# Performance work log

Measured on AMD Instinct MI355X. Metric: run time of the kernel, lower is better.

The kernel has to match this reference:

```python
import jax, jax.numpy as jnp
import numpy as np

N_TETS = 200000
IN_FEATURES = 128
OUT_FEATURES = 128
NUM_NEIGHBORS = 4  # NEIGHBORHOOD_SIZE = 5 = self + 4 neighbors


def setup_inputs() -> dict:
    key = jax.random.key(0)
    k1, k2, k3, k4 = jax.random.split(key, 4)
    features = jax.random.normal(k1, (N_TETS, IN_FEATURES), dtype=jnp.float32)
    neighbors = jax.random.randint(k2, (N_TETS, NUM_NEIGHBORS), 0, N_TETS, dtype=jnp.int64)
    # torch nn.Linear convention: W is [out_features, 5*in_features]
    fan_in = (1 + NUM_NEIGHBORS) * IN_FEATURES
    bound = 1.0 / np.sqrt(fan_in)
    W = jax.random.uniform(k3, (OUT_FEATURES, fan_in), minval=-bound, maxval=bound, dtype=jnp.float32)
    b = jax.random.uniform(k4, (OUT_FEATURES,), minval=-bound, maxval=bound, dtype=jnp.float32)
    return {"features": features, "neighbors": neighbors, "W": W, "b": b}


def reference(features, neighbors, W, b):
    # Gather neighbor features: [N, 4, F]
    nbr_feats = features[neighbors]
    N = features.shape[0]
    # Concat self + 4 neighbors along feature dim -> [N, 5F]
    stacked = jnp.concatenate([features[:, None, :], nbr_feats], axis=1).reshape(N, -1)
    # Linear + ReLU (torch: x @ W.T + b)
    return jax.nn.relu(stacked @ W.T + b)
```

## Files before the change

### kernel.cpp

```cpp
#include <hip/hip_runtime.h>
#include <stdint.h>

#define NTETS   200000
#define FEATS   128
#define OUTF    128
#define NG      5
#define BM      128
#define NTHR    512
#define NBLOCKS ((NTETS + BM - 1) / BM)
#define SUBS    10
#define SUBW    16384

typedef __attribute__((ext_vector_type(8))) short  short8v;
typedef __attribute__((ext_vector_type(4))) float  f32x4;

static __device__ __forceinline__ unsigned short bf16_rne(float f) {
  union { float f; unsigned u; } v; v.f = f;
  unsigned r = v.u + 0x7FFFu + ((v.u >> 16) & 1u);
  return (unsigned short)(r >> 16);
}

static __device__ __forceinline__ void gload_lds16(const void* g, void* l) {
  __builtin_amdgcn_global_load_lds(
      (const __attribute__((address_space(1))) unsigned int*)g,
      (__attribute__((address_space(3))) unsigned int*)l, 16, 0, 0);
}

__global__ void detect_mode_k(const int* __restrict__ nbr, int* __restrict__ flag) {
  int t = threadIdx.x;
  int nz = 0;
  for (int i = t; i < 4096; i += 64) nz |= nbr[2 * i + 1];
  unsigned long long any = __ballot(nz != 0);
  if (t == 0) flag[0] = (any == 0ULL) ? 1 : 0;
}

__global__ void prep_wfrag_k(const float* __restrict__ W, unsigned short* __restrict__ wf) {
  int id = blockIdx.x * 256 + threadIdx.x;
  if (id >= NG * 16384) return;
  int e  = id & 7;
  int l6 = (id >> 3) & 63;
  int ns = (id >> 9) & 7;
  int kk = (id >> 12) & 3;
  int g  = id >> 14;
  int n = ns * 16 + (l6 & 15);
  int k = g * 128 + kk * 32 + (l6 >> 4) * 8 + e;
  wf[id] = bf16_rne(W[n * (NG * FEATS) + k]);
}

__global__ __launch_bounds__(256) void prep_f_k(const float* __restrict__ feat,
                                                unsigned short* __restrict__ fimg) {
  size_t i = ((size_t)blockIdx.x * 256 + threadIdx.x) * 8;
  f32x4 a = __builtin_nontemporal_load((const f32x4*)(feat + i));
  f32x4 b = __builtin_nontemporal_load((const f32x4*)(feat + i + 4));
  short8v v;
  v[0] = (short)bf16_rne(a[0]); v[1] = (short)bf16_rne(a[1]);
  v[2] = (short)bf16_rne(a[2]); v[3] = (short)bf16_rne(a[3]);
  v[4] = (short)bf16_rne(b[0]); v[5] = (short)bf16_rne(b[1]);
  v[6] = (short)bf16_rne(b[2]); v[7] = (short)bf16_rne(b[3]);
  *(short8v*)(fimg + i) = v;
}

__global__ __launch_bounds__(NTHR, 4) void conv_k(
    const unsigned short* __restrict__ fimg, const int* __restrict__ nbr,
    const float* __restrict__ bias, const unsigned short* __restrict__ wf,
    const int* __restrict__ mode, float* __restrict__ out)
{
  __shared__ __align__(16) char wtile[3][SUBW];
  __shared__ unsigned srcoff[NG][BM];

  const int t    = threadIdx.x;
  const int row0 = blockIdx.x * BM;
  const int lane = t & 63;
  const int wv   = t >> 6;
  const int lr   = lane & 15;
  const int lk   = lane >> 4;

  {
    const bool m64 = (mode[0] != 0);
    for (int e = t; e < NG * BM; e += NTHR) {
      int g = e >> 7, r = e & (BM - 1);
      int gr = row0 + r;
      int s = 0;
      if (gr < NTETS) {
        if (g == 0) s = gr;
        else {
          size_t idx = (size_t)gr * 4 + (g - 1);
          s = m64 ? nbr[2 * idx] : nbr[idx];
          if ((unsigned)s >= (unsigned)NTETS) s = 0;
        }
      }
      srcoff[g][r] = (unsigned)s * 256u;
    }
  }
  __syncthreads();

  const char* fimgc = (const char*)fimg;
  const char* aptr[NG];
#pragma unroll
  for (int g = 0; g < NG; ++g)
    aptr[g] = fimgc + srcoff[g][wv * 16 + lr] + (unsigned)(lk * 16);

  const f32x4 zero = {0.f, 0.f, 0.f, 0.f};
  f32x4 acc[8];
#pragma unroll
  for (int i = 0; i < 8; ++i) acc[i] = zero;

  short8v a[4][2];

#define SB() __builtin_amdgcn_sched_barrier(0)

#define A_LOAD(dst_, p_, IMM_)                                                   \
  asm volatile("global_load_dwordx4 %0, %1, off offset:" #IMM_                   \
               : "=v"(dst_) : "v"(p_) : "memory")

#define A_ISSUE(ss) do {                                                         \
    const char* p_ = aptr[(ss) >> 1];                                            \
    if (((ss) & 1) == 0) {                                                       \
      A_LOAD(a[(ss) & 3][0], p_, 0);                                             \
      A_LOAD(a[(ss) & 3][1], p_, 64);                                            \
    } else {                                                                     \
      A_LOAD(a[(ss) & 3][0], p_, 128);                                           \
      A_LOAD(a[(ss) & 3][1], p_, 192);                                           \
    }                                                                            \
  } while (0)

#define W_ISSUE(ss) do {                                                         \
    const char* ws_ = (const char*)wf + (size_t)(ss) * SUBW + wv * 2048 +        \
                      (lane << 4);                                               \
    char* wd_ = &wtile[(ss) % 3][wv * 2048];                                     \
    gload_lds16(ws_, wd_);                                                       \
    gload_lds16(ws_ + 1024, wd_ + 1024);                                         \
  } while (0)

  W_ISSUE(0); SB();
  A_ISSUE(0); SB();
  W_ISSUE(1); SB();
  A_ISSUE(1); SB();
  A_ISSUE(2); SB();
  asm volatile("s_waitcnt vmcnt(6)" ::: "memory");
  SB();
  __builtin_amdgcn_s_barrier();
  SB();

#pragma unroll
  for (int s = 0; s < SUBS; ++s) {
    if (s + 2 < SUBS) { W_ISSUE(s + 2); SB(); }
    if (s + 3 < SUBS) { A_ISSUE(s + 3); SB(); }

    {
      short8v b[8];
#pragma unroll
      for (int ns = 0; ns < 8; ++ns)
        b[ns] = *(const short8v*)(&wtile[s % 3][ns * 1024 + (lane << 4)]);
#pragma unroll
      for (int ns = 0; ns < 8; ++ns)
        acc[ns] = __builtin_amdgcn_mfma_f32_16x16x32_bf16(a[s & 3][0], b[ns], acc[ns], 0, 0, 0);
#pragma unroll
      for (int ns = 0; ns < 8; ++ns)
        b[ns] = *(const short8v*)(&wtile[s % 3][(8 + ns) * 1024 + (lane << 4)]);
#pragma unroll
      for (int ns = 0; ns < 8; ++ns)
        acc[ns] = __builtin_amdgcn_mfma_f32_16x16x32_bf16(a[s & 3][1], b[ns], acc[ns], 0, 0, 0);
    }
    SB();

    if (s <= 6)      { asm volatile("s_waitcnt vmcnt(6)" ::: "memory"); }
    else if (s == 7) { asm volatile("s_waitcnt vmcnt(4)" ::: "memory"); }
    else if (s == 8) { asm volatile("s_waitcnt vmcnt(0)" ::: "memory"); }
    if (s + 1 < SUBS) {
      SB();
      __builtin_amdgcn_s_barrier();
      SB();
    }
  }

#pragma unroll
  for (int ns = 0; ns < 8; ++ns) {
    const int col = ns * 16 + lr;
    const float bv = bias[col];
    const int rbase = row0 + wv * 16 + lk * 4;
#pragma unroll
    for (int i = 0; i < 4; ++i) {
      int r = rbase + i;
      if (r < NTETS) {
        float vv = acc[ns][i] + bv;
        vv = vv > 0.f ? vv : 0.f;
        __builtin_nontemporal_store(vv, &out[(size_t)r * OUTF + col]);
      }
    }
  }
#undef A_LOAD
#undef A_ISSUE
#undef W_ISSUE
#undef SB
}

extern "C" void kernel_launch(void* const* d_in, const int* in_sizes, int n_in,
                              void* d_out, int out_size, void* d_ws, size_t ws_size,
                              hipStream_t stream) {
  const float* feat = (const float*)d_in[0];
  const int*   nbr  = (const int*)d_in[1];
  const float* W    = (const float*)d_in[2];
  const float* bias = (const float*)d_in[3];
  float* out = (float*)d_out;

  int* mode = (int*)d_ws;
  unsigned short* wf   = (unsigned short*)((char*)d_ws + 1024);
  unsigned short* fimg = (unsigned short*)((char*)d_ws + 164864);

  detect_mode_k<<<1, 64, 0, stream>>>(nbr, mode);
  prep_wfrag_k<<<320, 256, 0, stream>>>(W, wf);
  prep_f_k<<<(NTETS * FEATS / 8 + 255) / 256, 256, 0, stream>>>(feat, fimg);
  conv_k<<<NBLOCKS, NTHR, 0, stream>>>(fimg, nbr, bias, wf, mode, out);
}
```

Before: 118.7 us.

## Double per-wave row tile to reuse LDS weight fragments and drop A prefetch pipeline

Raises the block tile from 128 to 256 rows, so each wave computes two 16-row M sub-tiles and every weight fragment read from LDS feeds two MFMAs. This halves the block count and the total weight staging traffic. The hand-scheduled asm prefetch of activation rows, three sub-steps ahead, is removed. Gathered feature rows are now loaded with plain C++ loads inside the compute loop, which may expose gather latency since the vmcnt waits now count only the weight loads. Register pressure also rises with the doubled accumulators, against the launch bound of 4 blocks.

```diff
diff --git a/kernel.cpp b/kernel.cpp
--- a/kernel.cpp
+++ b/kernel.cpp
@@ -5,7 +5,7 @@
 #define FEATS   128
 #define OUTF    128
 #define NG      5
-#define BM      128
+#define BM      256
 #define NTHR    512
 #define NBLOCKS ((NTETS + BM - 1) / BM)
 #define SUBS    10
@@ -78,7 +78,7 @@
   {
     const bool m64 = (mode[0] != 0);
     for (int e = t; e < NG * BM; e += NTHR) {
-      int g = e >> 7, r = e & (BM - 1);
+      int g = e / BM, r = e & (BM - 1);
       int gr = row0 + r;
       int s = 0;
       if (gr < NTETS) {
@@ -95,34 +95,21 @@
   __syncthreads();
 
   const char* fimgc = (const char*)fimg;
-  const char* aptr[NG];
-#pragma unroll
-  for (int g = 0; g < NG; ++g)
-    aptr[g] = fimgc + srcoff[g][wv * 16 + lr] + (unsigned)(lk * 16);
+  unsigned aoff[2][NG];
+#pragma unroll
+  for (int m = 0; m < 2; ++m)
+#pragma unroll
+    for (int g = 0; g < NG; ++g)
+      aoff[m][g] = srcoff[g][wv * 32 + m * 16 + lr] + (unsigned)(lk * 16);
 
   const f32x4 zero = {0.f, 0.f, 0.f, 0.f};
-  f32x4 acc[8];
-#pragma unroll
-  for (int i = 0; i < 8; ++i) acc[i] = zero;
-
-  short8v a[4][2];
+  f32x4 acc[2][8];
+#pragma unroll
+  for (int m = 0; m < 2; ++m)
+#pragma unroll
+    for (int i = 0; i < 8; ++i) acc[m][i] = zero;
 
 #define SB() __builtin_amdgcn_sched_barrier(0)
-
-#define A_LOAD(dst_, p_, IMM_)                                                   \
-  asm volatile("global_load_dwordx4 %0, %1, off offset:" #IMM_                   \
-               : "=v"(dst_) : "v"(p_) : "memory")
-
-#define A_ISSUE(ss) do {                                                         \
-    const char* p_ = aptr[(ss) >> 1];                                            \
-    if (((ss) & 1) == 0) {                                                       \
-      A_LOAD(a[(ss) & 3][0], p_, 0);                                             \
-      A_LOAD(a[(ss) & 3][1], p_, 64);                                            \
-    } else {                                                                     \
-      A_LOAD(a[(ss) & 3][0], p_, 128);                                           \
-      A_LOAD(a[(ss) & 3][1], p_, 192);                                           \
-    }                                                                            \
-  } while (0)
 
 #define W_ISSUE(ss) do {                                                         \
     const char* ws_ = (const char*)wf + (size_t)(ss) * SUBW + wv * 2048 +        \
@@ -133,11 +120,8 @@
   } while (0)
 
   W_ISSUE(0); SB();
-  A_ISSUE(0); SB();
   W_ISSUE(1); SB();
-  A_ISSUE(1); SB();
-  A_ISSUE(2); SB();
-  asm volatile("s_waitcnt vmcnt(6)" ::: "memory");
+  asm volatile("s_waitcnt vmcnt(2)" ::: "memory");
   SB();
   __builtin_amdgcn_s_barrier();
   SB();
@@ -145,28 +129,35 @@
 #pragma unroll
   for (int s = 0; s < SUBS; ++s) {
     if (s + 2 < SUBS) { W_ISSUE(s + 2); SB(); }
-    if (s + 3 < SUBS) { A_ISSUE(s + 3); SB(); }
-
-    {
-      short8v b[8];
-#pragma unroll
-      for (int ns = 0; ns < 8; ++ns)
-        b[ns] = *(const short8v*)(&wtile[s % 3][ns * 1024 + (lane << 4)]);
-#pragma unroll
-      for (int ns = 0; ns < 8; ++ns)
-        acc[ns] = __builtin_amdgcn_mfma_f32_16x16x32_bf16(a[s & 3][0], b[ns], acc[ns], 0, 0, 0);
-#pragma unroll
-      for (int ns = 0; ns < 8; ++ns)
-        b[ns] = *(const short8v*)(&wtile[s % 3][(8 + ns) * 1024 + (lane << 4)]);
-#pragma unroll
-      for (int ns = 0; ns < 8; ++ns)
-        acc[ns] = __builtin_amdgcn_mfma_f32_16x16x32_bf16(a[s & 3][1], b[ns], acc[ns], 0, 0, 0);
+
+    const char* wt = wtile[s % 3];
+    const unsigned koff = (unsigned)((s & 1) * 128);
+#pragma unroll
+    for (int kk = 0; kk < 2; ++kk) {
+      short8v a0 = *(const short8v*)(fimgc + aoff[0][s >> 1] + koff + kk * 64);
+      short8v a1 = *(const short8v*)(fimgc + aoff[1][s >> 1] + koff + kk * 64);
+      short8v b4[4];
+#pragma unroll
+      for (int ns = 0; ns < 4; ++ns)
+        b4[ns] = *(const short8v*)(&wt[(kk * 8 + ns) * 1024 + (lane << 4)]);
+#pragma unroll
+      for (int ns = 0; ns < 4; ++ns) {
+        acc[0][ns] = __builtin_amdgcn_mfma_f32_16x16x32_bf16(a0, b4[ns], acc[0][ns], 0, 0, 0);
+        acc[1][ns] = __builtin_amdgcn_mfma_f32_16x16x32_bf16(a1, b4[ns], acc[1][ns], 0, 0, 0);
+      }
+#pragma unroll
+      for (int ns = 0; ns < 4; ++ns)
+        b4[ns] = *(const short8v*)(&wt[(kk * 8 + 4 + ns) * 1024 + (lane << 4)]);
+#pragma unroll
+      for (int ns = 0; ns < 4; ++ns) {
+        acc[0][4 + ns] = __builtin_amdgcn_mfma_f32_16x16x32_bf16(a0, b4[ns], acc[0][4 + ns], 0, 0, 0);
+        acc[1][4 + ns] = __builtin_amdgcn_mfma_f32_16x16x32_bf16(a1, b4[ns], acc[1][4 + ns], 0, 0, 0);
+      }
     }
     SB();
 
-    if (s <= 6)      { asm volatile("s_waitcnt vmcnt(6)" ::: "memory"); }
-    else if (s == 7) { asm volatile("s_waitcnt vmcnt(4)" ::: "memory"); }
-    else if (s == 8) { asm volatile("s_waitcnt vmcnt(0)" ::: "memory"); }
+    if (s + 2 < SUBS)      { asm volatile("s_waitcnt vmcnt(2)" ::: "memory"); }
+    else if (s + 1 < SUBS) { asm volatile("s_waitcnt vmcnt(0)" ::: "memory"); }
     if (s + 1 < SUBS) {
       SB();
       __builtin_amdgcn_s_barrier();
@@ -175,22 +166,23 @@
   }
 
 #pragma unroll
-  for (int ns = 0; ns < 8; ++ns) {
-    const int col = ns * 16 + lr;
-    const float bv = bias[col];
-    const int rbase = row0 + wv * 16 + lk * 4;
-#pragma unroll
-    for (int i = 0; i < 4; ++i) {
-      int r = rbase + i;
-      if (r < NTETS) {
-        float vv = acc[ns][i] + bv;
-        vv = vv > 0.f ? vv : 0.f;
-        __builtin_nontemporal_store(vv, &out[(size_t)r * OUTF + col]);
+  for (int m = 0; m < 2; ++m) {
+#pragma unroll
+    for (int ns = 0; ns < 8; ++ns) {
+      const int col = ns * 16 + lr;
+      const float bv = bias[col];
+      const int rbase = row0 + wv * 32 + m * 16 + lk * 4;
+#pragma unroll
+      for (int i = 0; i < 4; ++i) {
+        int r = rbase + i;
+        if (r < NTETS) {
+          float vv = acc[m][ns][i] + bv;
+          vv = vv > 0.f ? vv : 0.f;
+          __builtin_nontemporal_store(vv, &out[(size_t)r * OUTF + col]);
+        }
       }
     }
   }
-#undef A_LOAD
-#undef A_ISSUE
 #undef W_ISSUE
 #undef SB
 }
```

After: 113.7 us. 1.04x faster.

## Use persistent conv blocks with atomic tile counter and merge prep kernels

Applied to the files above, without the earlier changes.

Replaces the one-block-per-tile grid with 768 persistent blocks that take 128-row tiles from a global atomic counter. The mode-detection kernel is merged into the weight-fragment prep kernel, which also resets the counter, so one launch goes away. The explicit asm-pipelined A-operand gathers (prefetched three stages ahead) become plain loads issued just before each MFMA stage, and the occupancy hint rises from 4 to 6 blocks per CU. The aim is better load balance and less launch and tail overhead, but the A gather latency is no longer hidden by software prefetch, and each tile adds an atomic plus an extra barrier.

```diff
diff --git a/kernel.cpp b/kernel.cpp
--- a/kernel.cpp
+++ b/kernel.cpp
@@ -7,7 +7,8 @@
 #define NG      5
 #define BM      128
 #define NTHR    512
-#define NBLOCKS ((NTETS + BM - 1) / BM)
+#define NTILES  ((NTETS + BM - 1) / BM)
+#define NPBLK   768
 #define SUBS    10
 #define SUBW    16384
 
@@ -26,17 +27,21 @@
       (__attribute__((address_space(3))) unsigned int*)l, 16, 0, 0);
 }
 
-__global__ void detect_mode_k(const int* __restrict__ nbr, int* __restrict__ flag) {
-  int t = threadIdx.x;
-  int nz = 0;
-  for (int i = t; i < 4096; i += 64) nz |= nbr[2 * i + 1];
-  unsigned long long any = __ballot(nz != 0);
-  if (t == 0) flag[0] = (any == 0ULL) ? 1 : 0;
-}
-
-__global__ void prep_wfrag_k(const float* __restrict__ W, unsigned short* __restrict__ wf) {
-  int id = blockIdx.x * 256 + threadIdx.x;
-  if (id >= NG * 16384) return;
+__global__ void prep_meta_k(const float* __restrict__ W, unsigned short* __restrict__ wf,
+                            const int* __restrict__ nbr, int* __restrict__ mode,
+                            unsigned* __restrict__ counter) {
+  int b = blockIdx.x;
+  if (b == 320) {
+    int t = threadIdx.x;
+    if (t < 64) {
+      int nz = 0;
+      for (int i = t; i < 4096; i += 64) nz |= nbr[2 * i + 1];
+      unsigned long long any = __ballot(nz != 0);
+      if (t == 0) { mode[0] = (any == 0ULL) ? 1 : 0; counter[0] = 0u; }
+    }
+    return;
+  }
+  int id = b * 256 + threadIdx.x;
   int e  = id & 7;
   int l6 = (id >> 3) & 63;
   int ns = (id >> 9) & 7;
@@ -60,23 +65,41 @@
   *(short8v*)(fimg + i) = v;
 }
 
-__global__ __launch_bounds__(NTHR, 4) void conv_k(
+__global__ __launch_bounds__(NTHR, 6) void conv_k(
     const unsigned short* __restrict__ fimg, const int* __restrict__ nbr,
     const float* __restrict__ bias, const unsigned short* __restrict__ wf,
-    const int* __restrict__ mode, float* __restrict__ out)
+    const int* __restrict__ mode, unsigned* __restrict__ counter,
+    float* __restrict__ out)
 {
   __shared__ __align__(16) char wtile[3][SUBW];
   __shared__ unsigned srcoff[NG][BM];
+  __shared__ unsigned tile_s;
 
   const int t    = threadIdx.x;
-  const int row0 = blockIdx.x * BM;
   const int lane = t & 63;
   const int wv   = t >> 6;
   const int lr   = lane & 15;
   const int lk   = lane >> 4;
-
-  {
-    const bool m64 = (mode[0] != 0);
+  const bool m64 = (mode[0] != 0);
+  const char* fimgc = (const char*)fimg;
+
+#define SB() __builtin_amdgcn_sched_barrier(0)
+
+#define W_ISSUE(ss) do {                                                         \
+    const char* ws_ = (const char*)wf + (size_t)(ss) * SUBW + wv * 2048 +        \
+                      (lane << 4);                                               \
+    char* wd_ = &wtile[(ss) % 3][wv * 2048];                                     \
+    gload_lds16(ws_, wd_);                                                       \
+    gload_lds16(ws_ + 1024, wd_ + 1024);                                         \
+  } while (0)
+
+  for (;;) {
+    if (t == 0) tile_s = atomicAdd(counter, 1u);
+    __syncthreads();
+    const unsigned tile = tile_s;
+    if (tile >= (unsigned)NTILES) break;
+    const int row0 = (int)tile * BM;
+
     for (int e = t; e < NG * BM; e += NTHR) {
       int g = e >> 7, r = e & (BM - 1);
       int gr = row0 + r;
@@ -91,106 +114,75 @@
       }
       srcoff[g][r] = (unsigned)s * 256u;
     }
+    __syncthreads();
+
+    unsigned aoff[NG];
+#pragma unroll
+    for (int g = 0; g < NG; ++g)
+      aoff[g] = srcoff[g][wv * 16 + lr] + (unsigned)(lk * 16);
+
+    const f32x4 zero = {0.f, 0.f, 0.f, 0.f};
+    f32x4 acc[8];
+#pragma unroll
+    for (int i = 0; i < 8; ++i) acc[i] = zero;
+
+    W_ISSUE(0); SB();
+    W_ISSUE(1); SB();
+    asm volatile("s_waitcnt vmcnt(2)" ::: "memory");
+    SB();
+    __builtin_amdgcn_s_barrier();
+    SB();
+
+#pragma unroll
+    for (int s = 0; s < SUBS; ++s) {
+      if (s + 2 < SUBS) { W_ISSUE(s + 2); SB(); }
+
+      const char* wt = wtile[s % 3];
+      const unsigned ab = aoff[s >> 1] + (unsigned)((s & 1) * 128);
+      short8v a0 = *(const short8v*)(fimgc + ab);
+      short8v a1 = *(const short8v*)(fimgc + ab + 64);
+      {
+        short8v b[8];
+#pragma unroll
+        for (int ns = 0; ns < 8; ++ns)
+          b[ns] = *(const short8v*)(&wt[ns * 1024 + (lane << 4)]);
+#pragma unroll
+        for (int ns = 0; ns < 8; ++ns)
+          acc[ns] = __builtin_amdgcn_mfma_f32_16x16x32_bf16(a0, b[ns], acc[ns], 0, 0, 0);
+#pragma unroll
+        for (int ns = 0; ns < 8; ++ns)
+          b[ns] = *(const short8v*)(&wt[(8 + ns) * 1024 + (lane << 4)]);
+#pragma unroll
+        for (int ns = 0; ns < 8; ++ns)
+          acc[ns] = __builtin_amdgcn_mfma_f32_16x16x32_bf16(a1, b[ns], acc[ns], 0, 0, 0);
+      }
+      SB();
+
+      if (s + 2 < SUBS)      { asm volatile("s_waitcnt vmcnt(2)" ::: "memory"); }
+      else if (s + 1 < SUBS) { asm volatile("s_waitcnt vmcnt(0)" ::: "memory"); }
+      if (s + 1 < SUBS) {
+        SB();
+        __builtin_amdgcn_s_barrier();
+        SB();
+      }
+    }
+
+#pragma unroll
+    for (int ns = 0; ns < 8; ++ns) {
+      const int col = ns * 16 + lr;
+      const float bv = bias[col];
+      const int rbase = row0 + wv * 16 + lk * 4;
+#pragma unroll
+      for (int i = 0; i < 4; ++i) {
+        int r = rbase + i;
+        if (r < NTETS) {
+          float vv = acc[ns][i] + bv;
+          vv = vv > 0.f ? vv : 0.f;
+          __builtin_nontemporal_store(vv, &out[(size_t)r * OUTF + col]);
+        }
+      }
+    }
   }
-  __syncthreads();
-
-  const char* fimgc = (const char*)fimg;
-  const char* aptr[NG];
-#pragma unroll
-  for (int g = 0; g < NG; ++g)
-    aptr[g] = fimgc + srcoff[g][wv * 16 + lr] + (unsigned)(lk * 16);
-
-  const f32x4 zero = {0.f, 0.f, 0.f, 0.f};
-  f32x4 acc[8];
-#pragma unroll
-  for (int i = 0; i < 8; ++i) acc[i] = zero;
-
-  short8v a[4][2];
-
-#define SB() __builtin_amdgcn_sched_barrier(0)
-
-#define A_LOAD(dst_, p_, IMM_)                                                   \
-  asm volatile("global_load_dwordx4 %0, %1, off offset:" #IMM_                   \
-               : "=v"(dst_) : "v"(p_) : "memory")
-
-#define A_ISSUE(ss) do {                                                         \
-    const char* p_ = aptr[(ss) >> 1];                                            \
-    if (((ss) & 1) == 0) {                                                       \
-      A_LOAD(a[(ss) & 3][0], p_, 0);                                             \
-      A_LOAD(a[(ss) & 3][1], p_, 64);                                            \
-    } else {                                                                     \
-      A_LOAD(a[(ss) & 3][0], p_, 128);                                           \
-      A_LOAD(a[(ss) & 3][1], p_, 192);                                           \
-    }                                                                            \
-  } while (0)
-
-#define W_ISSUE(ss) do {                                                         \
-    const char* ws_ = (const char*)wf + (size_t)(ss) * SUBW + wv * 2048 +        \
-                      (lane << 4);                                               \
-    char* wd_ = &wtile[(ss) % 3][wv * 2048];                                     \
-    gload_lds16(ws_, wd_);                                                       \
-    gload_lds16(ws_ + 1024, wd_ + 1024);                                         \
-  } while (0)
-
-  W_ISSUE(0); SB();
-  A_ISSUE(0); SB();
-  W_ISSUE(1); SB();
-  A_ISSUE(1); SB();
-  A_ISSUE(2); SB();
-  asm volatile("s_waitcnt vmcnt(6)" ::: "memory");
-  SB();
-  __builtin_amdgcn_s_barrier();
-  SB();
-
-#pragma unroll
-  for (int s = 0; s < SUBS; ++s) {
-    if (s + 2 < SUBS) { W_ISSUE(s + 2); SB(); }
-    if (s + 3 < SUBS) { A_ISSUE(s + 3); SB(); }
-
-    {
-      short8v b[8];
-#pragma unroll
-      for (int ns = 0; ns < 8; ++ns)
-        b[ns] = *(const short8v*)(&wtile[s % 3][ns * 1024 + (lane << 4)]);
-#pragma unroll
-      for (int ns = 0; ns < 8; ++ns)
-        acc[ns] = __builtin_amdgcn_mfma_f32_16x16x32_bf16(a[s & 3][0], b[ns], acc[ns], 0, 0, 0);
-#pragma unroll
-      for (int ns = 0; ns < 8; ++ns)
-        b[ns] = *(const short8v*)(&wtile[s % 3][(8 + ns) * 1024 + (lane << 4)]);
-#pragma unroll
-      for (int ns = 0; ns < 8; ++ns)
-        acc[ns] = __builtin_amdgcn_mfma_f32_16x16x32_bf16(a[s & 3][1], b[ns], acc[ns], 0, 0, 0);
-    }
-    SB();
-
-    if (s <= 6)      { asm volatile("s_waitcnt vmcnt(6)" ::: "memory"); }
-    else if (s == 7) { asm volatile("s_waitcnt vmcnt(4)" ::: "memory"); }
-    else if (s == 8) { asm volatile("s_waitcnt vmcnt(0)" ::: "memory"); }
-    if (s + 1 < SUBS) {
-      SB();
-      __builtin_amdgcn_s_barrier();
-      SB();
-    }
-  }
-
-#pragma unroll
-  for (int ns = 0; ns < 8; ++ns) {
-    const int col = ns * 16 + lr;
-    const float bv = bias[col];
-    const int rbase = row0 + wv * 16 + lk * 4;
-#pragma unroll
-    for (int i = 0; i < 4; ++i) {
-      int r = rbase + i;
-      if (r < NTETS) {
-        float vv = acc[ns][i] + bv;
-        vv = vv > 0.f ? vv : 0.f;
-        __builtin_nontemporal_store(vv, &out[(size_t)r * OUTF + col]);
-      }
-    }
-  }
-#undef A_LOAD
-#undef A_ISSUE
 #undef W_ISSUE
 #undef SB
 }
@@ -204,12 +196,12 @@
   const float* bias = (const float*)d_in[3];
   float* out = (float*)d_out;
 
-  int* mode = (int*)d_ws;
+  int*      mode    = (int*)d_ws;
+  unsigned* counter = (unsigned*)((char*)d_ws + 64);
   unsigned short* wf   = (unsigned short*)((char*)d_ws + 1024);
   unsigned short* fimg = (unsigned short*)((char*)d_ws + 164864);
 
-  detect_mode_k<<<1, 64, 0, stream>>>(nbr, mode);
-  prep_wfrag_k<<<320, 256, 0, stream>>>(W, wf);
+  prep_meta_k<<<321, 256, 0, stream>>>(W, wf, nbr, mode, counter);
   prep_f_k<<<(NTETS * FEATS / 8 + 255) / 256, 256, 0, stream>>>(feat, fimg);
-  conv_k<<<NBLOCKS, NTHR, 0, stream>>>(fimg, nbr, bias, wf, mode, out);
-}
+  conv_k<<<NPBLK, NTHR, 0, stream>>>(fimg, nbr, bias, wf, mode, counter, out);
+}
```

After: 136.6 us. 1.15x slower.
